# Optimization experiments

Measured on AMD Instinct MI355X. Metric: run time of the kernel, lower is better.

## Reference

```python
import jax, jax.numpy as jnp
import numpy as np

B, C, Hs, Ws = 2, 256, 64, 64
NQ = Hs * Ws
NH, NP = 8, 8
N_CROSS, N_SELF = 2, 2
FFN = 256
DH = C // NH


def _layernorm(x, g, b, eps=1e-5):
    m = jnp.mean(x, -1, keepdims=True)
    v = jnp.mean((x - m) ** 2, -1, keepdims=True)
    return (x - m) * jax.lax.rsqrt(v + eps) * g + b


def _sine_pos_embed(h, w, num_feats=C // 2, temperature=10000.0):
    # SinePositionEmbedding(d_model//2, normalize=True) on an all-ones mask
    eps = 1e-6
    scale = 2.0 * np.pi
    y = jnp.arange(1, h + 1, dtype=jnp.float32) / (h + eps) * scale
    x = jnp.arange(1, w + 1, dtype=jnp.float32) / (w + eps) * scale
    dim_t = temperature ** (2.0 * (jnp.arange(num_feats) // 2).astype(jnp.float32) / num_feats)
    py = y[:, None] / dim_t  # [h, F]
    px = x[:, None] / dim_t  # [w, F]

    def interleave(p):
        return jnp.stack([jnp.sin(p[:, 0::2]), jnp.cos(p[:, 1::2])], -1).reshape(p.shape[0], -1)

    py = interleave(py)
    px = interleave(px)
    pos = jnp.concatenate([
        jnp.broadcast_to(py[:, None, :], (h, w, num_feats)),
        jnp.broadcast_to(px[None, :, :], (h, w, num_feats)),
    ], -1)
    return pos.reshape(h * w, 2 * num_feats)  # [hw, C]


def _msdeform(query, ref, src, ow, ob, aww, awb, vw, vb, pw, pb):
    # query [B,Lq,C], ref [B,Lq,2] (level dim of 1 squeezed), src [B,Len,C]
    Bq, Lq, _ = query.shape
    Len = src.shape[1]
    value = (src @ vw + vb).reshape(Bq, Len, NH, DH)
    off = (query @ ow + ob).reshape(Bq, Lq, NH, NP, 2)
    aw = jax.nn.softmax((query @ aww + awb).reshape(Bq, Lq, NH, NP), axis=-1)
    norm = jnp.array([Ws, Hs], jnp.float32)
    loc = ref[:, :, None, None, :] + off / norm  # [B,Lq,NH,NP,2], normalized coords
    # grid_sample bilinear, align_corners=False, zero padding
    px = loc[..., 0] * Ws - 0.5
    py = loc[..., 1] * Hs - 0.5
    x0 = jnp.floor(px)
    y0 = jnp.floor(py)
    lx, ly = px - x0, py - y0
    x0i = x0.astype(jnp.int32)
    y0i = y0.astype(jnp.int32)
    v = value.transpose(0, 2, 1, 3)  # [B,NH,Len,DH]

    def corner(xi, yi, w):
        inb = ((xi >= 0) & (xi < Ws) & (yi >= 0) & (yi < Hs)).astype(v.dtype)
        idx = jnp.clip(yi, 0, Hs - 1) * Ws + jnp.clip(xi, 0, Ws - 1)  # [B,Lq,NH,NP]
        idx = idx.transpose(0, 2, 1, 3).reshape(Bq, NH, Lq * NP)
        wT = (w * inb).transpose(0, 2, 1, 3).reshape(Bq, NH, Lq * NP, 1)
        g = jnp.take_along_axis(v, idx[..., None], axis=2)  # [B,NH,Lq*NP,DH]
        return g * wT

    s = (corner(x0i, y0i, (1 - lx) * (1 - ly))
         + corner(x0i + 1, y0i, lx * (1 - ly))
         + corner(x0i, y0i + 1, (1 - lx) * ly)
         + corner(x0i + 1, y0i + 1, lx * ly))  # [B,NH,Lq*NP,DH]
    s = s.reshape(Bq, NH, Lq, NP, DH)
    out = jnp.einsum('bqhp,bhqpd->bqhd', aw, s).reshape(Bq, Lq, C)
    return out @ pw + pb


def _ffn(x, w1, b1, w2, b2):
    return jax.nn.relu(jax.nn.relu(x @ w1 + b1) @ w2 + b2)


def setup_inputs() -> dict:
    key = jax.random.key(0)
    ks = jax.random.split(key, 16)
    s = 0.02
    return {
        'feat0': jax.random.normal(ks[0], (B, C, Hs, Ws), jnp.float32),
        'feat1': jax.random.normal(ks[1], (B, C, Hs, Ws), jnp.float32),
        'query_embed': jax.random.normal(ks[2], (NQ, 2 * C), jnp.float32),
        'ref_w': jax.random.normal(ks[3], (C, 2), jnp.float32) * s,
        'ref_b': jnp.zeros((2,), jnp.float32),
        'fuse_logit': jax.random.normal(ks[4], (2, C), jnp.float32) * s,
        'ln1_g': jnp.ones((4, C), jnp.float32),
        'ln1_b': jnp.zeros((4, C), jnp.float32),
        'off_w': jax.random.normal(ks[5], (4, C, NH * NP * 2), jnp.float32) * s,
        'off_b': jnp.zeros((4, NH * NP * 2), jnp.float32),
        'aw_w': jax.random.normal(ks[6], (4, C, NH * NP), jnp.float32) * s,
        'aw_b': jnp.zeros((4, NH * NP), jnp.float32),
        'val_w': jax.random.normal(ks[7], (4, C, C), jnp.float32) * s,
        'val_b': jnp.zeros((4, C), jnp.float32),
        'out_w': jax.random.normal(ks[8], (4, C, C), jnp.float32) * s,
        'out_b': jnp.zeros((4, C), jnp.float32),
        'ln2_g': jnp.ones((4, C), jnp.float32),
        'ln2_b': jnp.zeros((4, C), jnp.float32),
        'f1_w': jax.random.normal(ks[9], (4, C, FFN), jnp.float32) * s,
        'f1_b': jnp.zeros((4, FFN), jnp.float32),
        'f2_w': jax.random.normal(ks[10], (4, FFN, C), jnp.float32) * s,
        'f2_b': jnp.zeros((4, C), jnp.float32),
    }


def reference(feat0, feat1, query_embed, ref_w, ref_b, fuse_logit, ln1_g, ln1_b,
              off_w, off_b, aw_w, aw_b, val_w, val_b, out_w, out_b,
              ln2_g, ln2_b, f1_w, f1_b, f2_w, f2_b):
    # ModifiedCNW: adaptive per-channel weighted fusion of the two modality maps
    fw = jax.nn.softmax(fuse_logit, axis=0)  # [2, C]
    fused = feat0 * fw[0][None, :, None, None] + feat1 * fw[1][None, :, None, None]
    fused = fused.reshape(B, C, NQ).transpose(0, 2, 1)  # [B, HW, C]

    pos = jnp.broadcast_to(_sine_pos_embed(Hs, Ws)[None], (B, NQ, C))
    qe = jnp.broadcast_to(query_embed[:, :C][None], (B, NQ, C))
    tgt = jnp.broadcast_to(query_embed[:, C:][None], (B, NQ, C))
    ref_pts = jax.nn.sigmoid(qe @ ref_w + ref_b)  # [B, NQ, 2], normalized

    # self-attn reference points are PIXEL coordinates (faithful to source, unnormalized)
    ry, rx = jnp.meshgrid(jnp.linspace(0.5, Hs - 0.5, Hs), jnp.linspace(0.5, Ws - 0.5, Ws), indexing='ij')
    self_ref = jnp.broadcast_to(jnp.stack([rx.reshape(-1), ry.reshape(-1)], -1)[None], (B, NQ, 2))

    for i in range(N_CROSS):
        t2 = _layernorm(tgt, ln1_g[i], ln1_b[i])
        a = _msdeform(t2 + qe, ref_pts, fused, off_w[i], off_b[i], aw_w[i], aw_b[i],
                      val_w[i], val_b[i], out_w[i], out_b[i])
        tgt = tgt + a
        tgt = tgt + _ffn(_layernorm(tgt, ln2_g[i], ln2_b[i]), f1_w[i], f1_b[i], f2_w[i], f2_b[i])

    for j in range(N_SELF):
        i = N_CROSS + j
        # source computes norm1(tgt) but discards it in the self-attn branch
        a = _msdeform(tgt + pos, self_ref, tgt, off_w[i], off_b[i], aw_w[i], aw_b[i],
                      val_w[i], val_b[i], out_w[i], out_b[i])
        tgt = tgt + a
        tgt = tgt + _ffn(_layernorm(tgt, ln2_g[i], ln2_b[i]), f1_w[i], f1_b[i], f2_w[i], f2_b[i])
    return tgt
```

## Files before the change

kernel.cpp:

```cpp
#include <hip/hip_runtime.h>
#include <hip/hip_bf16.h>
#include <math.h>

#define CC   256
#define NQQ  4096
#define MT   8192

typedef __attribute__((ext_vector_type(8))) short s8v;
typedef __attribute__((ext_vector_type(4))) float f4v;

static __device__ __forceinline__ ushort f2bu(float f) {
    __hip_bfloat16 h = __float2bfloat16(f);
    return *reinterpret_cast<ushort*>(&h);
}


__global__ __launch_bounds__(256) void setup_kernel(
        const float* __restrict__ qemb, const float* __restrict__ rw,
        const float* __restrict__ rb,
        const float* __restrict__ feat0, const float* __restrict__ feat1,
        const float* __restrict__ fl,
        const float* __restrict__ val_w, const float* __restrict__ off_w,
        const float* __restrict__ aw_w,  const float* __restrict__ out_w,
        const float* __restrict__ f1_w,  const float* __restrict__ f2_w,
        const float* __restrict__ off_b, const float* __restrict__ aw_b,
        float* __restrict__ pos, float* __restrict__ refp, float* __restrict__ tgt,
        ushort* __restrict__ wval01, ushort* __restrict__ wvalS,
        ushort* __restrict__ woffaw, ushort* __restrict__ wout,
        ushort* __restrict__ wf1, ushort* __restrict__ wf2,
        float* __restrict__ bOA, ushort* __restrict__ fused) {
    __shared__ float tl[64][65];
    int bid = blockIdx.x;
    int t = threadIdx.x;
    if (bid < 2048) {
        int idx = bid * 256 + t;
        int q = idx >> 7, pp = idx & 127;
        int p = pp >> 6, u = pp & 63;
        float coordbase = (p == 0) ? (float)((q >> 6) + 1) : (float)((q & 63) + 1);
        float coord = coordbase * (6.28318530717958647692f / (64.0f + 1e-6f));
        float v = coord * exp2f(-0.20762050593046016f * (float)u);
        *(float2*)(pos + (size_t)q * 256 + p * 128 + u * 2) = make_float2(__sinf(v), __cosf(v));
        return;
    }
    if (bid < 3072) {
        int row = (bid - 2048) * 4 + (t >> 6);
        int l = t & 63;
        float4 v = *(const float4*)(qemb + (size_t)row * 512 + l * 4);
        float a0 = v.x * rw[(l * 4 + 0) * 2] + v.y * rw[(l * 4 + 1) * 2]
                 + v.z * rw[(l * 4 + 2) * 2] + v.w * rw[(l * 4 + 3) * 2];
        float a1 = v.x * rw[(l * 4 + 0) * 2 + 1] + v.y * rw[(l * 4 + 1) * 2 + 1]
                 + v.z * rw[(l * 4 + 2) * 2 + 1] + v.w * rw[(l * 4 + 3) * 2 + 1];
        #pragma unroll
        for (int o = 32; o > 0; o >>= 1) { a0 += __shfl_xor(a0, o); a1 += __shfl_xor(a1, o); }
        if (l == 0) {
            refp[row * 2 + 0] = 1.0f / (1.0f + __expf(-(a0 + rb[0])));
            refp[row * 2 + 1] = 1.0f / (1.0f + __expf(-(a1 + rb[1])));
        }
        return;
    }
    if (bid < 5120) {
        int idx = (bid - 3072) * 256 + t;
        int c4 = idx & 63;
        int q = (idx >> 6) & (NQQ - 1);
        *(float4*)(tgt + (size_t)idx * 4) = *(const float4*)(qemb + (size_t)q * 512 + 256 + c4 * 4);
        return;
    }
    if (bid < 5428) {
        int wb = bid - 5120;
        if (wb >= 304) {
            int layer = wb - 304;
            if (t < 192)
                bOA[layer * 192 + t] = (t < 128) ? off_b[layer * 128 + t]
                                                 : aw_b[layer * 64 + (t - 128)];
            return;
        }
        const float* src; ushort* dstF; int srcStride, ntb, kcb;
        if (wb < 32) {
            int nt = wb & 7, kt = wb >> 3;
            int layer = nt >> 2, nn = (nt & 3) * 64;
            src = val_w + (size_t)layer * 65536 + (size_t)kt * 64 * 256 + nn; srcStride = 256;
            dstF = wval01; ntb = nt * 4; kcb = kt * 2;
        } else if (wb < 64) {
            int b = wb - 32; int layer = b >> 4; int kt = (b >> 2) & 3; int nt = b & 3;
            src = val_w + (size_t)(2 + layer) * 65536 + (size_t)kt * 64 * 256 + nt * 64; srcStride = 256;
            dstF = wvalS + (size_t)layer * 65536; ntb = nt * 4; kcb = kt * 2;
        } else if (wb < 112) {
            int b = wb - 64; int layer = b / 12; int rem = b % 12; int kt = rem / 3; int nt = rem % 3;
            if (nt < 2) { src = off_w + (size_t)layer * 256 * 128 + (size_t)kt * 64 * 128 + nt * 64; srcStride = 128; }
            else        { src = aw_w  + (size_t)layer * 256 * 64  + (size_t)kt * 64 * 64;            srcStride = 64;  }
            dstF = woffaw + (size_t)layer * 49152; ntb = nt * 4; kcb = kt * 2;
        } else {
            int b = wb - 112; int fam = b >> 6; int bb = b & 63;
            int layer = bb >> 4; int kt = (bb >> 2) & 3; int nt = bb & 3;
            const float* s0 = (fam == 0) ? out_w : ((fam == 1) ? f1_w : f2_w);
            ushort* d0      = (fam == 0) ? wout  : ((fam == 1) ? wf1  : wf2);
            src = s0 + (size_t)layer * 65536 + (size_t)kt * 64 * 256 + nt * 64; srcStride = 256;
            dstF = d0 + (size_t)layer * 65536; ntb = nt * 4; kcb = kt * 2;
        }
        int r = t >> 6, c = t & 63;
        #pragma unroll
        for (int rr = 0; rr < 64; rr += 4)
            tl[rr + r][c] = src[(size_t)(rr + r) * srcStride + c];
        __syncthreads();
        int l = t >> 2;
        int e0 = (t & 3) * 2;
        int frow = l & 15;
        int fcol = (l >> 4) * 8;
        #pragma unroll
        for (int s = 0; s < 8; s++) {
            int ntl = s & 3, kcl = s >> 2;
            int ntile = ntb + ntl, kc = kcb + kcl;
            ushort2 val;
            val.x = f2bu(tl[kcl * 32 + fcol + e0    ][ntl * 16 + frow]);
            val.y = f2bu(tl[kcl * 32 + fcol + e0 + 1][ntl * 16 + frow]);
            *(ushort2*)(dstF + (((size_t)ntile * 8 + kc) * 64 + l) * 8 + e0) = val;
        }
        return;
    }
    {
        int fb = bid - 5428;
        int b = fb >> 8;
        int c0 = ((fb >> 6) & 3) * 64;
        int q0 = (fb & 63) * 64;
        int r = t >> 6, c = t & 63;
        #pragma unroll
        for (int rr = 0; rr < 64; rr += 4) {
            int ch = c0 + rr + r;
            float l0 = fl[ch], l1 = fl[CC + ch];
            float m = fmaxf(l0, l1);
            float e0 = __expf(l0 - m), e1 = __expf(l1 - m);
            float inv = 1.0f / (e0 + e1);
            size_t o = ((size_t)b * CC + ch) * NQQ + q0 + c;
            tl[rr + r][c] = (feat0[o] * e0 + feat1[o] * e1) * inv;
        }
        __syncthreads();
        #pragma unroll
        for (int rr = 0; rr < 64; rr += 4)
            fused[((size_t)(b * NQQ + q0 + rr + r)) * CC + c0 + c] = f2bu(tl[c][rr + r]);
    }
}

template<int ASRC, int NTJ>
__global__ __launch_bounds__(512) void pgemm(const ushort* __restrict__ Abf,
        const float* __restrict__ Af, const ushort* __restrict__ Wf,
        const float* __restrict__ bias, ushort* __restrict__ Cb, int NS) {
    __shared__ ushort Abuf[16 * 264];
    const int t = threadIdx.x;
    const int m0 = blockIdx.x * 16;
    const int cb0 = blockIdx.y * 256;
    const int ntb = blockIdx.y * 16;
    {
        const int rg = t >> 5, c0 = (t & 31) * 8;
        ushort* dst = Abuf + rg * 264 + c0;
        if (ASRC == 0) {
            *(int4*)dst = *(const int4*)(Abf + (size_t)(m0 + rg) * 256 + c0);
        } else {
            const float* src = Af + (size_t)(m0 + rg) * 256 + c0;
            ushort tmp[8];
            #pragma unroll
            for (int j = 0; j < 2; j++) {
                float4 v = *(const float4*)(src + j * 4);
                tmp[j * 4 + 0] = f2bu(v.x); tmp[j * 4 + 1] = f2bu(v.y);
                tmp[j * 4 + 2] = f2bu(v.z); tmp[j * 4 + 3] = f2bu(v.w);
            }
            *(int4*)dst = *(const int4*)tmp;
        }
    }
    __syncthreads();
    const int l = t & 63, w = t >> 6;
    const int fr = l & 15, fk8 = (l >> 4) * 8, rb = (l >> 4) * 4;
    f4v acc[NTJ] = {};
    #pragma unroll
    for (int kc = 0; kc < 8; kc++) {
        s8v a = *(const s8v*)(Abuf + fr * 264 + kc * 32 + fk8);
        #pragma unroll
        for (int j = 0; j < NTJ; j++) {
            int nt = ntb + j * 8 + w;
            s8v b = *(const s8v*)(Wf + (((size_t)nt * 8 + kc) * 64 + l) * 8);
            acc[j] = __builtin_amdgcn_mfma_f32_16x16x32_bf16(a, b, acc[j], 0, 0, 0);
        }
    }
    #pragma unroll
    for (int j = 0; j < NTJ; j++) {
        int gcol = cb0 + (j * 8 + w) * 16 + fr;
        float bz = bias[gcol];
        #pragma unroll
        for (int r = 0; r < 4; r++)
            Cb[(size_t)(m0 + rb + r) * NS + gcol] = f2bu(acc[j][r] + bz);
    }
}

template<int SELF, int EMITVAL>
__global__ __launch_bounds__(512) void layer_kernel(
        float* __restrict__ tgt, const float* __restrict__ posq,
        const float* __restrict__ g1, const float* __restrict__ b1,
        const ushort* __restrict__ woffawL, const float* __restrict__ bOAL,
        const ushort* __restrict__ value, int vstride,
        const float* __restrict__ refp,
        const ushort* __restrict__ woutL, const float* __restrict__ out_bL,
        const float* __restrict__ g2, const float* __restrict__ b2,
        const ushort* __restrict__ wf1L, const float* __restrict__ f1_bL,
        const ushort* __restrict__ wf2L, const float* __restrict__ f2_bL,
        const ushort* __restrict__ wvalN, const float* __restrict__ val_bN,
        ushort* __restrict__ valueOut) {
    __shared__ ushort Abuf[16 * 264];
    __shared__ float Slds[16 * 204];
    __shared__ float pred[2][8][16];
    const int t = threadIdx.x;
    const int m0 = blockIdx.x * 16;

    {
        const int rg = t >> 5, c0 = (t & 31) * 8;
        int m = m0 + rg, q = m & (NQQ - 1);
        const float* src = tgt + (size_t)m * 256 + c0;
        float fv[8];
        *(float4*)&fv[0] = *(const float4*)src;
        *(float4*)&fv[4] = *(const float4*)(src + 4);
        if (!SELF) {
            float s = 0.0f;
            #pragma unroll
            for (int k = 0; k < 8; k++) s += fv[k];
            s += __shfl_xor(s, 1); s += __shfl_xor(s, 2); s += __shfl_xor(s, 4);
            s += __shfl_xor(s, 8); s += __shfl_xor(s, 16);
            float mean = s * (1.0f / 256.0f);
            float s2 = 0.0f;
            #pragma unroll
            for (int k = 0; k < 8; k++) { float d = fv[k] - mean; s2 += d * d; }
            s2 += __shfl_xor(s2, 1); s2 += __shfl_xor(s2, 2); s2 += __shfl_xor(s2, 4);
            s2 += __shfl_xor(s2, 8); s2 += __shfl_xor(s2, 16);
            float rstd = rsqrtf(s2 * (1.0f / 256.0f) + 1e-5f);
            const float* ep = posq + (size_t)q * 512 + c0;
            #pragma unroll
            for (int k = 0; k < 8; k++)
                fv[k] = (fv[k] - mean) * rstd * g1[c0 + k] + b1[c0 + k] + ep[k];
        } else {
            const float* ep = posq + (size_t)q * 256 + c0;
            #pragma unroll
            for (int k = 0; k < 8; k++) fv[k] += ep[k];
        }
        ushort tmp[8];
        #pragma unroll
        for (int k = 0; k < 8; k++) tmp[k] = f2bu(fv[k]);
        *(int4*)(Abuf + rg * 264 + c0) = *(const int4*)tmp;
    }
    __syncthreads();

    const int l = t & 63, w = t >> 6;
    const int fr = l & 15, fk8 = (l >> 4) * 8, rb = (l >> 4) * 4;

    {
        f4v oacc[2] = {};
        #pragma unroll
        for (int kc = 0; kc < 8; kc++) {
            s8v a = *(const s8v*)(Abuf + fr * 264 + kc * 32 + fk8);
            #pragma unroll
            for (int j = 0; j < 2; j++) {
                int nt = j * 8 + w;
                if (nt < 12) {
                    s8v b = *(const s8v*)(woffawL + (((size_t)nt * 8 + kc) * 64 + l) * 8);
                    oacc[j] = __builtin_amdgcn_mfma_f32_16x16x32_bf16(a, b, oacc[j], 0, 0, 0);
                }
            }
        }
        #pragma unroll
        for (int j = 0; j < 2; j++) {
            int nt = j * 8 + w;
            if (nt < 12) {
                int gcol = nt * 16 + fr;
                float bz = bOAL[gcol];
                #pragma unroll
                for (int r = 0; r < 4; r++)
                    Slds[(rb + r) * 204 + gcol] = oacc[j][r] + bz;
            }
        }
    }
    __syncthreads();

    {
        const int row = t >> 5, h = (t >> 2) & 7, d8 = t & 3;
        int m = m0 + row, q = m & (NQQ - 1), bidx = m >> 12;
        float rxs, rys;
        if (SELF) { rxs = (float)(q & 63) * 64.0f + 32.0f; rys = (float)(q >> 6) * 64.0f + 32.0f; }
        else      { rxs = refp[q * 2] * 64.0f;             rys = refp[q * 2 + 1] * 64.0f; }
        const float* oa = Slds + row * 204;
        float lg[8];
        #pragma unroll
        for (int p = 0; p < 8; p++) lg[p] = oa[128 + h * 8 + p];
        float mx = lg[0];
        #pragma unroll
        for (int p = 1; p < 8; p++) mx = fmaxf(mx, lg[p]);
        float wg[8], wsum = 0.0f;
        #pragma unroll
        for (int p = 0; p < 8; p++) { wg[p] = __expf(lg[p] - mx); wsum += wg[p]; }
        float inv = 1.0f / wsum;
        const float* offp = oa + h * 16;
        const ushort* vb = value + (size_t)bidx * NQQ * vstride + h * 32 + d8 * 8;
        float acc[8] = {};
        #pragma unroll
        for (int p = 0; p < 8; p++) {
            float px = rxs + offp[p * 2]     - 0.5f;
            float py = rys + offp[p * 2 + 1] - 0.5f;
            float x0f = floorf(px), y0f = floorf(py);
            float lx = px - x0f, ly = py - y0f;
            int x0 = (int)x0f, y0 = (int)y0f;
            float wgt = wg[p] * inv;
            float w00 = (1 - lx) * (1 - ly) * wgt, w10 = lx * (1 - ly) * wgt;
            float w01 = (1 - lx) * ly * wgt,       w11 = lx * ly * wgt;
            #pragma unroll
            for (int cn = 0; cn < 4; cn++) {
                int xi = x0 + (cn & 1), yi = y0 + (cn >> 1);
                float wc = (cn == 0) ? w00 : (cn == 1) ? w10 : (cn == 2) ? w01 : w11;
                if (xi >= 0 && xi < 64 && yi >= 0 && yi < 64) {
                    uint4 uv = *(const uint4*)(vb + (size_t)(yi * 64 + xi) * vstride);
                    uint ua[4] = {uv.x, uv.y, uv.z, uv.w};
                    #pragma unroll
                    for (int k = 0; k < 4; k++) {
                        uint lo = ua[k] << 16;
                        uint hi = ua[k] & 0xffff0000u;
                        acc[k * 2 + 0] += wc * *reinterpret_cast<float*>(&lo);
                        acc[k * 2 + 1] += wc * *reinterpret_cast<float*>(&hi);
                    }
                }
            }
        }
        ushort pk[8];
        #pragma unroll
        for (int k = 0; k < 8; k++) pk[k] = f2bu(acc[k]);
        *(int4*)(Abuf + row * 264 + h * 32 + d8 * 8) = *(const int4*)pk;
    }
    __syncthreads();

    float v[4][2];
    {
        f4v acc[2] = {};
        #pragma unroll
        for (int kc = 0; kc < 8; kc++) {
            s8v a = *(const s8v*)(Abuf + fr * 264 + kc * 32 + fk8);
            #pragma unroll
            for (int j = 0; j < 2; j++) {
                int nt = j * 8 + w;
                s8v b = *(const s8v*)(woutL + (((size_t)nt * 8 + kc) * 64 + l) * 8);
                acc[j] = __builtin_amdgcn_mfma_f32_16x16x32_bf16(a, b, acc[j], 0, 0, 0);
            }
        }
        float ls[4] = {}, lq[4] = {};
        #pragma unroll
        for (int j = 0; j < 2; j++) {
            int gcol = (j * 8 + w) * 16 + fr;
            float bz = out_bL[gcol];
            #pragma unroll
            for (int r = 0; r < 4; r++) {
                float tv = tgt[(size_t)(m0 + rb + r) * 256 + gcol] + acc[j][r] + bz;
                v[r][j] = tv;
                ls[r] += tv;
                lq[r] += tv * tv;
            }
        }
        #pragma unroll
        for (int o = 1; o < 16; o <<= 1)
            #pragma unroll
            for (int r = 0; r < 4; r++) {
                ls[r] += __shfl_xor(ls[r], o);
                lq[r] += __shfl_xor(lq[r], o);
            }
        if (fr == 0)
            #pragma unroll
            for (int r = 0; r < 4; r++) {
                pred[0][w][rb + r] = ls[r];
                pred[1][w][rb + r] = lq[r];
            }
    }
    __syncthreads();

    #pragma unroll
    for (int r = 0; r < 4; r++) {
        int rloc = rb + r;
        float s = 0.0f, sq = 0.0f;
        #pragma unroll
        for (int ww = 0; ww < 8; ww++) { s += pred[0][ww][rloc]; sq += pred[1][ww][rloc]; }
        float mean = s * (1.0f / 256.0f);
        float var = sq * (1.0f / 256.0f) - mean * mean;
        float rstd = rsqrtf(var + 1e-5f);
        #pragma unroll
        for (int j = 0; j < 2; j++) {
            int gcol = (j * 8 + w) * 16 + fr;
            Abuf[rloc * 264 + gcol] = f2bu((v[r][j] - mean) * rstd * g2[gcol] + b2[gcol]);
        }
    }
    __syncthreads();

    {
        f4v acc[2] = {};
        #pragma unroll
        for (int kc = 0; kc < 8; kc++) {
            s8v a = *(const s8v*)(Abuf + fr * 264 + kc * 32 + fk8);
            #pragma unroll
            for (int j = 0; j < 2; j++) {
                int nt = j * 8 + w;
                s8v b = *(const s8v*)(wf1L + (((size_t)nt * 8 + kc) * 64 + l) * 8);
                acc[j] = __builtin_amdgcn_mfma_f32_16x16x32_bf16(a, b, acc[j], 0, 0, 0);
            }
        }
        __syncthreads();
        #pragma unroll
        for (int j = 0; j < 2; j++) {
            int gcol = (j * 8 + w) * 16 + fr;
            float bz = f1_bL[gcol];
            #pragma unroll
            for (int r = 0; r < 4; r++)
                Abuf[(rb + r) * 264 + gcol] = f2bu(fmaxf(acc[j][r] + bz, 0.0f));
        }
    }
    __syncthreads();

    {
        f4v acc[2] = {};
        #pragma unroll
        for (int kc = 0; kc < 8; kc++) {
            s8v a = *(const s8v*)(Abuf + fr * 264 + kc * 32 + fk8);
            #pragma unroll
            for (int j = 0; j < 2; j++) {
                int nt = j * 8 + w;
                s8v b = *(const s8v*)(wf2L + (((size_t)nt * 8 + kc) * 64 + l) * 8);
                acc[j] = __builtin_amdgcn_mfma_f32_16x16x32_bf16(a, b, acc[j], 0, 0, 0);
            }
        }
        if (EMITVAL) __syncthreads();
        #pragma unroll
        for (int j = 0; j < 2; j++) {
            int gcol = (j * 8 + w) * 16 + fr;
            float bz = f2_bL[gcol];
            #pragma unroll
            for (int r = 0; r < 4; r++) {
                float fin = v[r][j] + fmaxf(acc[j][r] + bz, 0.0f);
                tgt[(size_t)(m0 + rb + r) * 256 + gcol] = fin;
                if (EMITVAL) Abuf[(rb + r) * 264 + gcol] = f2bu(fin);
            }
        }
    }
    if (EMITVAL) {
        __syncthreads();
        f4v acc[2] = {};
        #pragma unroll
        for (int kc = 0; kc < 8; kc++) {
            s8v a = *(const s8v*)(Abuf + fr * 264 + kc * 32 + fk8);
            #pragma unroll
            for (int j = 0; j < 2; j++) {
                int nt = j * 8 + w;
                s8v b = *(const s8v*)(wvalN + (((size_t)nt * 8 + kc) * 64 + l) * 8);
                acc[j] = __builtin_amdgcn_mfma_f32_16x16x32_bf16(a, b, acc[j], 0, 0, 0);
            }
        }
        #pragma unroll
        for (int j = 0; j < 2; j++) {
            int gcol = (j * 8 + w) * 16 + fr;
            float bz = val_bN[gcol];
            #pragma unroll
            for (int r = 0; r < 4; r++)
                valueOut[(size_t)(m0 + rb + r) * 256 + gcol] = f2bu(acc[j][r] + bz);
        }
    }
}

extern "C" void kernel_launch(void* const* d_in, const int* in_sizes, int n_in,
                              void* d_out, int out_size, void* d_ws, size_t ws_size,
                              hipStream_t stream) {
    const float* feat0 = (const float*)d_in[0];
    const float* feat1 = (const float*)d_in[1];
    const float* qemb  = (const float*)d_in[2];
    const float* ref_w = (const float*)d_in[3];
    const float* ref_b = (const float*)d_in[4];
    const float* fl    = (const float*)d_in[5];
    const float* ln1_g = (const float*)d_in[6];
    const float* ln1_b = (const float*)d_in[7];
    const float* off_w = (const float*)d_in[8];
    const float* off_b = (const float*)d_in[9];
    const float* aw_w  = (const float*)d_in[10];
    const float* aw_b  = (const float*)d_in[11];
    const float* val_w = (const float*)d_in[12];
    const float* val_b = (const float*)d_in[13];
    const float* out_w = (const float*)d_in[14];
    const float* out_b = (const float*)d_in[15];
    const float* ln2_g = (const float*)d_in[16];
    const float* ln2_b = (const float*)d_in[17];
    const float* f1_w  = (const float*)d_in[18];
    const float* f1_b  = (const float*)d_in[19];
    const float* f2_w  = (const float*)d_in[20];
    const float* f2_b  = (const float*)d_in[21];

    float* tgt = (float*)d_out;
    float* ws = (float*)d_ws;
    float* pos     = ws;
    float* refp    = pos + 1048576;
    float* bOA     = refp + 8192;
    ushort* value01= (ushort*)(bOA + 768);
    ushort* valueS0= value01 + (size_t)MT * 512;
    ushort* valueS1= valueS0 + (size_t)MT * 256;
    ushort* wval01 = valueS1 + (size_t)MT * 256;
    ushort* wvalS  = wval01 + 131072;
    ushort* woffaw = wvalS + 131072;
    ushort* wout   = woffaw + 196608;
    ushort* wf1    = wout + 262144;
    ushort* wf2    = wf1 + 262144;
    ushort* fused_bf = wf2 + 262144;

    setup_kernel<<<5940, 256, 0, stream>>>(qemb, ref_w, ref_b, feat0, feat1, fl,
                                           val_w, off_w, aw_w, out_w, f1_w, f2_w,
                                           off_b, aw_b,
                                           pos, refp, tgt,
                                           wval01, wvalS, woffaw, wout, wf1, wf2,
                                           bOA, fused_bf);

    pgemm<0, 2><<<dim3(512, 2), 512, 0, stream>>>(fused_bf, nullptr, wval01, val_b, value01, 512);

    layer_kernel<0, 0><<<512, 512, 0, stream>>>(
        tgt, qemb, ln1_g, ln1_b,
        woffaw, bOA, value01, 512, refp,
        wout, out_b, ln2_g, ln2_b,
        wf1, f1_b, wf2, f2_b,
        nullptr, nullptr, nullptr);
    layer_kernel<0, 1><<<512, 512, 0, stream>>>(
        tgt, qemb, ln1_g + CC, ln1_b + CC,
        woffaw + 49152, bOA + 192, value01 + 256, 512, refp,
        wout + 65536, out_b + CC, ln2_g + CC, ln2_b + CC,
        wf1 + 65536, f1_b + CC, wf2 + 65536, f2_b + CC,
        wvalS, val_b + 2 * CC, valueS0);
    layer_kernel<1, 1><<<512, 512, 0, stream>>>(
        tgt, pos, nullptr, nullptr,
        woffaw + 2 * 49152, bOA + 2 * 192, valueS0, 256, refp,
        wout + 2 * 65536, out_b + 2 * CC, ln2_g + 2 * CC, ln2_b + 2 * CC,
        wf1 + 2 * 65536, f1_b + 2 * CC, wf2 + 2 * 65536, f2_b + 2 * CC,
        wvalS + 65536, val_b + 3 * CC, valueS1);
    layer_kernel<1, 0><<<512, 512, 0, stream>>>(
        tgt, pos, nullptr, nullptr,
        woffaw + 3 * 49152, bOA + 3 * 192, valueS1, 256, refp,
        wout + 3 * 65536, out_b + 3 * CC, ln2_g + 3 * CC, ln2_b + 3 * CC,
        wf1 + 3 * 65536, f1_b + 3 * CC, wf2 + 3 * 65536, f2_b + 3 * CC,
        nullptr, nullptr, nullptr);
}
```

Before: 137.0 us.

## Process 32 rows per block with 16 waves each owning one column tile

Blocks in the GEMM and fused layer kernels now handle 32 query rows with 1024 threads instead of 16 rows with 512. Each wave owns a single 16-column output tile and reuses its loaded weight fragment across two row groups, halving per-row weight fetch traffic. The post-attention LayerNorm reduction moves to a per-row pass over 16 wave partials through shared memory, which adds a barrier. Grid size halves to 256 blocks, so fewer blocks may underfill the CUs, and LDS per block doubles.

```diff
diff --git a/kernel.cpp b/kernel.cpp
--- a/kernel.cpp
+++ b/kernel.cpp
@@ -140,58 +140,41 @@
     }
 }
 
-template<int ASRC, int NTJ>
-__global__ __launch_bounds__(512) void pgemm(const ushort* __restrict__ Abf,
-        const float* __restrict__ Af, const ushort* __restrict__ Wf,
-        const float* __restrict__ bias, ushort* __restrict__ Cb, int NS) {
-    __shared__ ushort Abuf[16 * 264];
+__global__ __launch_bounds__(1024, 4) void pgemm(const ushort* __restrict__ Abf,
+        const ushort* __restrict__ Wf, const float* __restrict__ bias,
+        ushort* __restrict__ Cb, int NS) {
+    __shared__ ushort Abuf[32 * 264];
     const int t = threadIdx.x;
-    const int m0 = blockIdx.x * 16;
+    const int m0 = blockIdx.x * 32;
     const int cb0 = blockIdx.y * 256;
     const int ntb = blockIdx.y * 16;
     {
         const int rg = t >> 5, c0 = (t & 31) * 8;
-        ushort* dst = Abuf + rg * 264 + c0;
-        if (ASRC == 0) {
-            *(int4*)dst = *(const int4*)(Abf + (size_t)(m0 + rg) * 256 + c0);
-        } else {
-            const float* src = Af + (size_t)(m0 + rg) * 256 + c0;
-            ushort tmp[8];
-            #pragma unroll
-            for (int j = 0; j < 2; j++) {
-                float4 v = *(const float4*)(src + j * 4);
-                tmp[j * 4 + 0] = f2bu(v.x); tmp[j * 4 + 1] = f2bu(v.y);
-                tmp[j * 4 + 2] = f2bu(v.z); tmp[j * 4 + 3] = f2bu(v.w);
-            }
-            *(int4*)dst = *(const int4*)tmp;
-        }
+        *(int4*)(Abuf + rg * 264 + c0) = *(const int4*)(Abf + (size_t)(m0 + rg) * 256 + c0);
     }
     __syncthreads();
     const int l = t & 63, w = t >> 6;
     const int fr = l & 15, fk8 = (l >> 4) * 8, rb = (l >> 4) * 4;
-    f4v acc[NTJ] = {};
+    f4v acc[2] = {};
     #pragma unroll
     for (int kc = 0; kc < 8; kc++) {
-        s8v a = *(const s8v*)(Abuf + fr * 264 + kc * 32 + fk8);
-        #pragma unroll
-        for (int j = 0; j < NTJ; j++) {
-            int nt = ntb + j * 8 + w;
-            s8v b = *(const s8v*)(Wf + (((size_t)nt * 8 + kc) * 64 + l) * 8);
-            acc[j] = __builtin_amdgcn_mfma_f32_16x16x32_bf16(a, b, acc[j], 0, 0, 0);
-        }
-    }
+        s8v b = *(const s8v*)(Wf + (((size_t)(ntb + w) * 8 + kc) * 64 + l) * 8);
+        s8v a0 = *(const s8v*)(Abuf + fr * 264 + kc * 32 + fk8);
+        s8v a1 = *(const s8v*)(Abuf + (16 + fr) * 264 + kc * 32 + fk8);
+        acc[0] = __builtin_amdgcn_mfma_f32_16x16x32_bf16(a0, b, acc[0], 0, 0, 0);
+        acc[1] = __builtin_amdgcn_mfma_f32_16x16x32_bf16(a1, b, acc[1], 0, 0, 0);
+    }
+    int gcol = cb0 + w * 16 + fr;
+    float bz = bias[gcol];
     #pragma unroll
-    for (int j = 0; j < NTJ; j++) {
-        int gcol = cb0 + (j * 8 + w) * 16 + fr;
-        float bz = bias[gcol];
+    for (int g = 0; g < 2; g++)
         #pragma unroll
         for (int r = 0; r < 4; r++)
-            Cb[(size_t)(m0 + rb + r) * NS + gcol] = f2bu(acc[j][r] + bz);
-    }
+            Cb[(size_t)(m0 + g * 16 + rb + r) * NS + gcol] = f2bu(acc[g][r] + bz);
 }
 
 template<int SELF, int EMITVAL>
-__global__ __launch_bounds__(512) void layer_kernel(
+__global__ __launch_bounds__(1024, 4) void layer_kernel(
         float* __restrict__ tgt, const float* __restrict__ posq,
         const float* __restrict__ g1, const float* __restrict__ b1,
         const ushort* __restrict__ woffawL, const float* __restrict__ bOAL,
@@ -203,11 +186,12 @@
         const ushort* __restrict__ wf2L, const float* __restrict__ f2_bL,
         const ushort* __restrict__ wvalN, const float* __restrict__ val_bN,
         ushort* __restrict__ valueOut) {
-    __shared__ ushort Abuf[16 * 264];
-    __shared__ float Slds[16 * 204];
-    __shared__ float pred[2][8][16];
+    __shared__ ushort Abuf[32 * 264];
+    __shared__ float Slds[32 * 204];
+    __shared__ float pred[2][16][32];
+    __shared__ float mrs[2][32];
     const int t = threadIdx.x;
-    const int m0 = blockIdx.x * 16;
+    const int m0 = blockIdx.x * 32;
 
     {
         const int rg = t >> 5, c0 = (t & 31) * 8;
@@ -248,31 +232,23 @@
     const int l = t & 63, w = t >> 6;
     const int fr = l & 15, fk8 = (l >> 4) * 8, rb = (l >> 4) * 4;
 
-    {
+    if (w < 12) {
         f4v oacc[2] = {};
         #pragma unroll
         for (int kc = 0; kc < 8; kc++) {
-            s8v a = *(const s8v*)(Abuf + fr * 264 + kc * 32 + fk8);
-            #pragma unroll
-            for (int j = 0; j < 2; j++) {
-                int nt = j * 8 + w;
-                if (nt < 12) {
-                    s8v b = *(const s8v*)(woffawL + (((size_t)nt * 8 + kc) * 64 + l) * 8);
-                    oacc[j] = __builtin_amdgcn_mfma_f32_16x16x32_bf16(a, b, oacc[j], 0, 0, 0);
-                }
-            }
-        }
-        #pragma unroll
-        for (int j = 0; j < 2; j++) {
-            int nt = j * 8 + w;
-            if (nt < 12) {
-                int gcol = nt * 16 + fr;
-                float bz = bOAL[gcol];
-                #pragma unroll
-                for (int r = 0; r < 4; r++)
-                    Slds[(rb + r) * 204 + gcol] = oacc[j][r] + bz;
-            }
-        }
+            s8v b = *(const s8v*)(woffawL + (((size_t)w * 8 + kc) * 64 + l) * 8);
+            s8v a0 = *(const s8v*)(Abuf + fr * 264 + kc * 32 + fk8);
+            s8v a1 = *(const s8v*)(Abuf + (16 + fr) * 264 + kc * 32 + fk8);
+            oacc[0] = __builtin_amdgcn_mfma_f32_16x16x32_bf16(a0, b, oacc[0], 0, 0, 0);
+            oacc[1] = __builtin_amdgcn_mfma_f32_16x16x32_bf16(a1, b, oacc[1], 0, 0, 0);
+        }
+        int gcol = w * 16 + fr;
+        float bz = bOAL[gcol];
+        #pragma unroll
+        for (int g = 0; g < 2; g++)
+            #pragma unroll
+            for (int r = 0; r < 4; r++)
+                Slds[(g * 16 + rb + r) * 204 + gcol] = oacc[g][r] + bz;
     }
     __syncthreads();
 
@@ -330,135 +306,127 @@
     }
     __syncthreads();
 
-    float v[4][2];
+    const int gcol = w * 16 + fr;
+
+    float v[2][4];
     {
         f4v acc[2] = {};
         #pragma unroll
         for (int kc = 0; kc < 8; kc++) {
-            s8v a = *(const s8v*)(Abuf + fr * 264 + kc * 32 + fk8);
-            #pragma unroll
-            for (int j = 0; j < 2; j++) {
-                int nt = j * 8 + w;
-                s8v b = *(const s8v*)(woutL + (((size_t)nt * 8 + kc) * 64 + l) * 8);
-                acc[j] = __builtin_amdgcn_mfma_f32_16x16x32_bf16(a, b, acc[j], 0, 0, 0);
+            s8v b = *(const s8v*)(woutL + (((size_t)w * 8 + kc) * 64 + l) * 8);
+            s8v a0 = *(const s8v*)(Abuf + fr * 264 + kc * 32 + fk8);
+            s8v a1 = *(const s8v*)(Abuf + (16 + fr) * 264 + kc * 32 + fk8);
+            acc[0] = __builtin_amdgcn_mfma_f32_16x16x32_bf16(a0, b, acc[0], 0, 0, 0);
+            acc[1] = __builtin_amdgcn_mfma_f32_16x16x32_bf16(a1, b, acc[1], 0, 0, 0);
+        }
+        float ls[2][4], lq[2][4];
+        float bz = out_bL[gcol];
+        #pragma unroll
+        for (int g = 0; g < 2; g++)
+            #pragma unroll
+            for (int r = 0; r < 4; r++) {
+                float tv = tgt[(size_t)(m0 + g * 16 + rb + r) * 256 + gcol] + acc[g][r] + bz;
+                v[g][r] = tv;
+                ls[g][r] = tv;
+                lq[g][r] = tv * tv;
             }
-        }
-        float ls[4] = {}, lq[4] = {};
-        #pragma unroll
-        for (int j = 0; j < 2; j++) {
-            int gcol = (j * 8 + w) * 16 + fr;
-            float bz = out_bL[gcol];
-            #pragma unroll
-            for (int r = 0; r < 4; r++) {
-                float tv = tgt[(size_t)(m0 + rb + r) * 256 + gcol] + acc[j][r] + bz;
-                v[r][j] = tv;
-                ls[r] += tv;
-                lq[r] += tv * tv;
-            }
-        }
         #pragma unroll
         for (int o = 1; o < 16; o <<= 1)
             #pragma unroll
-            for (int r = 0; r < 4; r++) {
-                ls[r] += __shfl_xor(ls[r], o);
-                lq[r] += __shfl_xor(lq[r], o);
-            }
+            for (int g = 0; g < 2; g++)
+                #pragma unroll
+                for (int r = 0; r < 4; r++) {
+                    ls[g][r] += __shfl_xor(ls[g][r], o);
+                    lq[g][r] += __shfl_xor(lq[g][r], o);
+                }
         if (fr == 0)
             #pragma unroll
-            for (int r = 0; r < 4; r++) {
-                pred[0][w][rb + r] = ls[r];
-                pred[1][w][rb + r] = lq[r];
-            }
-    }
-    __syncthreads();
-
-    #pragma unroll
-    for (int r = 0; r < 4; r++) {
-        int rloc = rb + r;
+            for (int g = 0; g < 2; g++)
+                #pragma unroll
+                for (int r = 0; r < 4; r++) {
+                    pred[0][w][g * 16 + rb + r] = ls[g][r];
+                    pred[1][w][g * 16 + rb + r] = lq[g][r];
+                }
+    }
+    __syncthreads();
+    if (t < 32) {
         float s = 0.0f, sq = 0.0f;
         #pragma unroll
-        for (int ww = 0; ww < 8; ww++) { s += pred[0][ww][rloc]; sq += pred[1][ww][rloc]; }
+        for (int ww = 0; ww < 16; ww++) { s += pred[0][ww][t]; sq += pred[1][ww][t]; }
         float mean = s * (1.0f / 256.0f);
         float var = sq * (1.0f / 256.0f) - mean * mean;
-        float rstd = rsqrtf(var + 1e-5f);
-        #pragma unroll
-        for (int j = 0; j < 2; j++) {
-            int gcol = (j * 8 + w) * 16 + fr;
-            Abuf[rloc * 264 + gcol] = f2bu((v[r][j] - mean) * rstd * g2[gcol] + b2[gcol]);
-        }
-    }
+        mrs[0][t] = mean;
+        mrs[1][t] = rsqrtf(var + 1e-5f);
+    }
+    __syncthreads();
+
+    #pragma unroll
+    for (int g = 0; g < 2; g++)
+        #pragma unroll
+        for (int r = 0; r < 4; r++) {
+            int rloc = g * 16 + rb + r;
+            Abuf[rloc * 264 + gcol] = f2bu((v[g][r] - mrs[0][rloc]) * mrs[1][rloc] * g2[gcol] + b2[gcol]);
+        }
     __syncthreads();
 
     {
         f4v acc[2] = {};
         #pragma unroll
         for (int kc = 0; kc < 8; kc++) {
-            s8v a = *(const s8v*)(Abuf + fr * 264 + kc * 32 + fk8);
-            #pragma unroll
-            for (int j = 0; j < 2; j++) {
-                int nt = j * 8 + w;
-                s8v b = *(const s8v*)(wf1L + (((size_t)nt * 8 + kc) * 64 + l) * 8);
-                acc[j] = __builtin_amdgcn_mfma_f32_16x16x32_bf16(a, b, acc[j], 0, 0, 0);
+            s8v b = *(const s8v*)(wf1L + (((size_t)w * 8 + kc) * 64 + l) * 8);
+            s8v a0 = *(const s8v*)(Abuf + fr * 264 + kc * 32 + fk8);
+            s8v a1 = *(const s8v*)(Abuf + (16 + fr) * 264 + kc * 32 + fk8);
+            acc[0] = __builtin_amdgcn_mfma_f32_16x16x32_bf16(a0, b, acc[0], 0, 0, 0);
+            acc[1] = __builtin_amdgcn_mfma_f32_16x16x32_bf16(a1, b, acc[1], 0, 0, 0);
+        }
+        __syncthreads();
+        float bz = f1_bL[gcol];
+        #pragma unroll
+        for (int g = 0; g < 2; g++)
+            #pragma unroll
+            for (int r = 0; r < 4; r++)
+                Abuf[(g * 16 + rb + r) * 264 + gcol] = f2bu(fmaxf(acc[g][r] + bz, 0.0f));
+    }
+    __syncthreads();
+
+    {
+        f4v acc[2] = {};
+        #pragma unroll
+        for (int kc = 0; kc < 8; kc++) {
+            s8v b = *(const s8v*)(wf2L + (((size_t)w * 8 + kc) * 64 + l) * 8);
+            s8v a0 = *(const s8v*)(Abuf + fr * 264 + kc * 32 + fk8);
+            s8v a1 = *(const s8v*)(Abuf + (16 + fr) * 264 + kc * 32 + fk8);
+            acc[0] = __builtin_amdgcn_mfma_f32_16x16x32_bf16(a0, b, acc[0], 0, 0, 0);
+            acc[1] = __builtin_amdgcn_mfma_f32_16x16x32_bf16(a1, b, acc[1], 0, 0, 0);
+        }
+        if (EMITVAL) __syncthreads();
+        float bz = f2_bL[gcol];
+        #pragma unroll
+        for (int g = 0; g < 2; g++)
+            #pragma unroll
+            for (int r = 0; r < 4; r++) {
+                float fin = v[g][r] + fmaxf(acc[g][r] + bz, 0.0f);
+                tgt[(size_t)(m0 + g * 16 + rb + r) * 256 + gcol] = fin;
+                if (EMITVAL) Abuf[(g * 16 + rb + r) * 264 + gcol] = f2bu(fin);
             }
-        }
-        __syncthreads();
-        #pragma unroll
-        for (int j = 0; j < 2; j++) {
-            int gcol = (j * 8 + w) * 16 + fr;
-            float bz = f1_bL[gcol];
-            #pragma unroll
-            for (int r = 0; r < 4; r++)
-                Abuf[(rb + r) * 264 + gcol] = f2bu(fmaxf(acc[j][r] + bz, 0.0f));
-        }
-    }
-    __syncthreads();
-
-    {
-        f4v acc[2] = {};
-        #pragma unroll
-        for (int kc = 0; kc < 8; kc++) {
-            s8v a = *(const s8v*)(Abuf + fr * 264 + kc * 32 + fk8);
-            #pragma unroll
-            for (int j = 0; j < 2; j++) {
-                int nt = j * 8 + w;
-                s8v b = *(const s8v*)(wf2L + (((size_t)nt * 8 + kc) * 64 + l) * 8);
-                acc[j] = __builtin_amdgcn_mfma_f32_16x16x32_bf16(a, b, acc[j], 0, 0, 0);
-            }
-        }
-        if (EMITVAL) __syncthreads();
-        #pragma unroll
-        for (int j = 0; j < 2; j++) {
-            int gcol = (j * 8 + w) * 16 + fr;
-            float bz = f2_bL[gcol];
-            #pragma unroll
-            for (int r = 0; r < 4; r++) {
-                float fin = v[r][j] + fmaxf(acc[j][r] + bz, 0.0f);
-                tgt[(size_t)(m0 + rb + r) * 256 + gcol] = fin;
-                if (EMITVAL) Abuf[(rb + r) * 264 + gcol] = f2bu(fin);
-            }
-        }
     }
     if (EMITVAL) {
         __syncthreads();
         f4v acc[2] = {};
         #pragma unroll
         for (int kc = 0; kc < 8; kc++) {
-            s8v a = *(const s8v*)(Abuf + fr * 264 + kc * 32 + fk8);
-            #pragma unroll
-            for (int j = 0; j < 2; j++) {
-                int nt = j * 8 + w;
-                s8v b = *(const s8v*)(wvalN + (((size_t)nt * 8 + kc) * 64 + l) * 8);
-                acc[j] = __builtin_amdgcn_mfma_f32_16x16x32_bf16(a, b, acc[j], 0, 0, 0);
-            }
-        }
-        #pragma unroll
-        for (int j = 0; j < 2; j++) {
-            int gcol = (j * 8 + w) * 16 + fr;
-            float bz = val_bN[gcol];
+            s8v b = *(const s8v*)(wvalN + (((size_t)w * 8 + kc) * 64 + l) * 8);
+            s8v a0 = *(const s8v*)(Abuf + fr * 264 + kc * 32 + fk8);
+            s8v a1 = *(const s8v*)(Abuf + (16 + fr) * 264 + kc * 32 + fk8);
+            acc[0] = __builtin_amdgcn_mfma_f32_16x16x32_bf16(a0, b, acc[0], 0, 0, 0);
+            acc[1] = __builtin_amdgcn_mfma_f32_16x16x32_bf16(a1, b, acc[1], 0, 0, 0);
+        }
+        float bz = val_bN[gcol];
+        #pragma unroll
+        for (int g = 0; g < 2; g++)
             #pragma unroll
             for (int r = 0; r < 4; r++)
-                valueOut[(size_t)(m0 + rb + r) * 256 + gcol] = f2bu(acc[j][r] + bz);
-        }
+                valueOut[(size_t)(m0 + g * 16 + rb + r) * 256 + gcol] = f2bu(acc[g][r] + bz);
     }
 }
 
@@ -511,27 +479,27 @@
                                            wval01, wvalS, woffaw, wout, wf1, wf2,
                                            bOA, fused_bf);
 
-    pgemm<0, 2><<<dim3(512, 2), 512, 0, stream>>>(fused_bf, nullptr, wval01, val_b, value01, 512);
-
-    layer_kernel<0, 0><<<512, 512, 0, stream>>>(
+    pgemm<<<dim3(256, 2), 1024, 0, stream>>>(fused_bf, wval01, val_b, value01, 512);
+
+    layer_kernel<0, 0><<<256, 1024, 0, stream>>>(
         tgt, qemb, ln1_g, ln1_b,
         woffaw, bOA, value01, 512, refp,
         wout, out_b, ln2_g, ln2_b,
         wf1, f1_b, wf2, f2_b,
         nullptr, nullptr, nullptr);
-    layer_kernel<0, 1><<<512, 512, 0, stream>>>(
+    layer_kernel<0, 1><<<256, 1024, 0, stream>>>(
         tgt, qemb, ln1_g + CC, ln1_b + CC,
         woffaw + 49152, bOA + 192, value01 + 256, 512, refp,
         wout + 65536, out_b + CC, ln2_g + CC, ln2_b + CC,
         wf1 + 65536, f1_b + CC, wf2 + 65536, f2_b + CC,
         wvalS, val_b + 2 * CC, valueS0);
-    layer_kernel<1, 1><<<512, 512, 0, stream>>>(
+    layer_kernel<1, 1><<<256, 1024, 0, stream>>>(
         tgt, pos, nullptr, nullptr,
         woffaw + 2 * 49152, bOA + 2 * 192, valueS0, 256, refp,
         wout + 2 * 65536, out_b + 2 * CC, ln2_g + 2 * CC, ln2_b + 2 * CC,
         wf1 + 2 * 65536, f1_b + 2 * CC, wf2 + 2 * 65536, f2_b + 2 * CC,
         wvalS + 65536, val_b + 3 * CC, valueS1);
-    layer_kernel<1, 0><<<512, 512, 0, stream>>>(
+    layer_kernel<1, 0><<<256, 1024, 0, stream>>>(
         tgt, pos, nullptr, nullptr,
         woffaw + 3 * 49152, bOA + 3 * 192, valueS1, 256, refp,
         wout + 3 * 65536, out_b + 3 * CC, ln2_g + 3 * CC, ln2_b + 3 * CC,
```

Measured after the change: 115.9 us. -15.4%, faster.
